# Optimization experiments

Measured on AMD Instinct MI355X. Metric: run time of the kernel, lower is better.

Reference implementation:

```python
import jax, jax.numpy as jnp
import numpy as np

DIM, HEADS = 1024, 16
B, N = 2, 2048


def setup_inputs() -> dict:
    key = jax.random.key(0)
    ks = jax.random.split(key, 8)
    d = DIM // HEADS
    return {
        "x": jax.random.normal(ks[0], (B, N, DIM), dtype=jnp.float32),
        "w_qkv": jax.random.normal(ks[1], (DIM, 3 * DIM), dtype=jnp.float32) * (DIM ** -0.5),
        "w_out": jax.random.normal(ks[2], (DIM, DIM), dtype=jnp.float32) * (DIM ** -0.5),
        "b_out": jnp.zeros((DIM,), dtype=jnp.float32),
        "void_q": jax.random.normal(ks[3], (1, HEADS, 1, d), dtype=jnp.float32),
        "void_k": jax.random.normal(ks[4], (1, HEADS, 1, d), dtype=jnp.float32),
        "void_v": jax.random.normal(ks[5], (1, HEADS, 1, d), dtype=jnp.float32),
        "attention_trace": jax.random.uniform(ks[6], (HEADS, 1, 1), dtype=jnp.float32),
        "temperature_factor": jax.random.normal(ks[7], (HEADS, 1, 1), dtype=jnp.float32),
    }


def reference(x, w_qkv, w_out, b_out, void_q, void_k, void_v,
              attention_trace, temperature_factor):
    b, n, dim = x.shape
    h = void_q.shape[1]
    d = dim // h

    qkv = x @ w_qkv  # [b, n, 3*dim]
    q, k, v = jnp.split(qkv, 3, axis=-1)

    def to_heads(t):
        return t.reshape(b, n, h, d).transpose(0, 2, 1, 3)  # b h n d

    q, k, v = to_heads(q), to_heads(k), to_heads(v)

    # append the void token to q, k, v -> seq length n+1
    q = jnp.concatenate([q, jnp.broadcast_to(void_q, (b, h, 1, d))], axis=2)
    k = jnp.concatenate([k, jnp.broadcast_to(void_k, (b, h, 1, d))], axis=2)
    v = jnp.concatenate([v, jnp.broadcast_to(void_v, (b, h, 1, d))], axis=2)

    # NOTE: original scales by full dim**-0.5, not head-dim
    dots = jnp.einsum('bhid,bhjd->bhij', q, k) * (dim ** -0.5)
    # void-to-void bias of +10 at index [n, n]
    dots = dots.at[:, :, n, n].add(10.0)

    # stateful per-head temperature (trace is a buffer, treated as input)
    temperature = jnp.maximum(1.0 + jnp.abs(attention_trace) * temperature_factor, 1.0)  # [h,1,1]
    attn = jax.nn.softmax(dots / temperature, axis=-1)  # [b, h, n+1, n+1]

    out = jnp.einsum('bhij,bhjd->bhid', attn, v)[:, :, :n, :]  # drop void row
    out = out.transpose(0, 2, 1, 3).reshape(b, n, dim)  # b n (h d)
    return out @ w_out + b_out
```

## Files before the change

### kernel.cpp

```cpp
#include <hip/hip_runtime.h>
#include <stdint.h>

#define DIMF   1024
#define HEADS  16
#define HD     64
#define BB     2
#define NN     2048
#define NKP    2112
#define NTILE  33

typedef __attribute__((ext_vector_type(8))) __bf16 bf16x8;
typedef __attribute__((ext_vector_type(4))) float  f32x4;

__device__ __forceinline__ float b2f(uint16_t h) {
  union { uint32_t u; float f; } v; v.u = ((uint32_t)h) << 16; return v.f;
}
__device__ __forceinline__ uint16_t f2b(float f) {
  union { float f; uint32_t u; } v; v.f = f;
  uint32_t r = v.u + 0x7FFFu + ((v.u >> 16) & 1u);
  return (uint16_t)(r >> 16);
}

__device__ __forceinline__ void gl_lds16(const void* g, void* l) {
  __builtin_amdgcn_global_load_lds(
      (const __attribute__((address_space(1))) void*)g,
      (__attribute__((address_space(3))) void*)l, 16, 0, 0);
}

__global__ __launch_bounds__(256) void prep_k(const float* __restrict__ x,
                                              uint16_t* __restrict__ x_bf,
                                              const float* __restrict__ vk,
                                              const float* __restrict__ vv,
                                              uint16_t* __restrict__ k_ws,
                                              uint16_t* __restrict__ vt_ws) {
  if (blockIdx.x < 4096) {
    int i = blockIdx.x * 256 + threadIdx.x;
    float4 v = *(const float4*)&x[(size_t)i * 4];
    uint16_t* d = x_bf + (size_t)i * 4;
    d[0] = f2b(v.x); d[1] = f2b(v.y); d[2] = f2b(v.z); d[3] = f2b(v.w);
  } else {
    int idx = (blockIdx.x - 4096) * 256 + threadIdx.x;
    int dd = idx & 63;
    int r  = (idx >> 6) & 63;
    int bh = idx >> 12;
    int h  = bh & (HEADS - 1);
    uint16_t kv  = (r == 0) ? f2b(vk[h * HD + dd]) : (uint16_t)0;
    uint16_t vvv = (r == 0) ? f2b(vv[h * HD + dd]) : (uint16_t)0;
    k_ws[((size_t)bh * NKP + NN + r) * HD + dd]  = kv;
    vt_ws[((size_t)bh * HD + dd) * NKP + NN + r] = vvv;
  }
}

__global__ __launch_bounds__(256) void transpose2_k(const float* __restrict__ w1,
                                                    uint16_t* __restrict__ d1,
                                                    const float* __restrict__ w2,
                                                    uint16_t* __restrict__ d2) {
  const int z = blockIdx.z;
  if (z == 1 && blockIdx.x >= 32) return;
  const float* src = z ? w2 : w1;
  uint16_t*   dst = z ? d2 : d1;
  const int M = 1024, N = z ? 1024 : 3072;
  __shared__ uint16_t tile[32][33];
  int bx = blockIdx.x * 32, by = blockIdx.y * 32;
  int x = threadIdx.x & 31, y0 = (threadIdx.x >> 5) * 4;
#pragma unroll
  for (int i = 0; i < 4; ++i)
    tile[y0 + i][x] = f2b(src[(size_t)(by + y0 + i) * N + bx + x]);
  __syncthreads();
#pragma unroll
  for (int i = 0; i < 4; ++i)
    dst[(size_t)(bx + y0 + i) * M + by + x] = tile[x][y0 + i];
}

template<int EPI>
__global__ __launch_bounds__(256) void gemm_bt(const uint16_t* __restrict__ A,
                                               const uint16_t* __restrict__ Bt,
                                               int K, int Nout,
                                               uint16_t* __restrict__ o0,
                                               uint16_t* __restrict__ o1,
                                               uint16_t* __restrict__ o2,
                                               float* __restrict__ fo,
                                               const float* __restrict__ bias) {
  __shared__ uint16_t lds_a[128][32];
  __shared__ uint16_t lds_b[128][32];
  const int m0 = blockIdx.y * 128, n0 = blockIdx.x * 128;
  const int tid = threadIdx.x, lane = tid & 63, wid = tid >> 6;
  const int wm = (wid >> 1) * 64, wn = (wid & 1) * 64;
  const int lr = lane & 15, lg = lane >> 4;
  f32x4 acc[4][4] = {};
  for (int k0 = 0; k0 < K; k0 += 32) {
    __syncthreads();
#pragma unroll
    for (int it = 0; it < 2; ++it) {
      const int chunk = wid * 2 + it;
      const int o = chunk * 1024 + lane * 16;
      const int r = o >> 6, cb = o & 63;
      gl_lds16((const char*)&A[(size_t)(m0 + r) * K + k0] + cb,
               (char*)&lds_a[0][0] + chunk * 1024);
      gl_lds16((const char*)&Bt[(size_t)(n0 + r) * K + k0] + cb,
               (char*)&lds_b[0][0] + chunk * 1024);
    }
    __syncthreads();
    bf16x8 af[4], bf[4];
#pragma unroll
    for (int i = 0; i < 4; ++i)
      af[i] = *(const bf16x8*)((const char*)&lds_a[0][0] + (wm + i * 16 + lr) * 64 + lg * 16);
#pragma unroll
    for (int j = 0; j < 4; ++j)
      bf[j] = *(const bf16x8*)((const char*)&lds_b[0][0] + (wn + j * 16 + lr) * 64 + lg * 16);
#pragma unroll
    for (int i = 0; i < 4; ++i)
#pragma unroll
      for (int j = 0; j < 4; ++j)
        acc[i][j] = __builtin_amdgcn_mfma_f32_16x16x32_bf16(af[i], bf[j], acc[i][j], 0, 0, 0);
  }
#pragma unroll
  for (int i = 0; i < 4; ++i)
#pragma unroll
    for (int j = 0; j < 4; ++j)
#pragma unroll
      for (int r = 0; r < 4; ++r) {
        int mg = m0 + wm + i * 16 + lg * 4 + r;
        int ng = n0 + wn + j * 16 + lr;
        float v = acc[i][j][r];
        if (EPI == 0) {
          int b = mg >> 11, n = mg & (NN - 1);
          int which = ng >> 10, rem = ng & (DIMF - 1), h = rem >> 6, dd = rem & 63;
          int bh = b * HEADS + h;
          uint16_t bv = f2b(v);
          if (which == 0)      o0[((size_t)bh * NN + n) * HD + dd] = bv;
          else if (which == 1) o1[((size_t)bh * NKP + n) * HD + dd] = bv;
          else                 o2[((size_t)bh * HD + dd) * NKP + n] = bv;
        } else {
          fo[(size_t)mg * Nout + ng] = v + bias[ng];
        }
      }
}

__global__ __launch_bounds__(256) void attn_k(const uint16_t* __restrict__ q_ws,
                                              const uint16_t* __restrict__ k_ws,
                                              const uint16_t* __restrict__ vt_ws,
                                              const float* __restrict__ trace,
                                              const float* __restrict__ factor,
                                              uint16_t* __restrict__ o_ws) {
  __shared__ uint16_t ldsk[64][64];
  __shared__ uint16_t ldsv[64][64];
  __shared__ uint16_t ldsp[4][16][72];
  const int bh = blockIdx.x;
  const int qb = blockIdx.y;
  const int h = bh & (HEADS - 1), b = bh >> 4;
  const int tid = threadIdx.x, lane = tid & 63, wid = tid >> 6;
  const int lr = lane & 15, lg = lane >> 4;

  const float temp  = fmaxf(1.0f + fabsf(trace[h]) * factor[h], 1.0f);
  const float scale = 0.03125f / temp;

  const int qrow0 = qb * 64 + wid * 16;
  const uint16_t* qrow = q_ws + ((size_t)bh * NN + qrow0 + lr) * HD;
  bf16x8 qf[2];
  qf[0] = *(const bf16x8*)(qrow + lg * 8);
  qf[1] = *(const bf16x8*)(qrow + 32 + lg * 8);

  const int rsw = (lr & 7) << 4;
  const char* kb0 = (const char*)&ldsk[0][0] + lr * 128 + ((lg * 16) ^ rsw);
  const char* kb1 = (const char*)&ldsk[0][0] + lr * 128 + ((64 + lg * 16) ^ rsw);
  const char* vb0 = (const char*)&ldsv[0][0] + lr * 128 + ((lg * 16) ^ rsw);
  const char* vb1 = (const char*)&ldsv[0][0] + lr * 128 + ((64 + lg * 16) ^ rsw);
  const char* pr  = (const char*)&ldsp[wid][lr][lg * 8];

  f32x4 acc[4] = {};
  float lsum[4] = {0.f, 0.f, 0.f, 0.f};

  for (int t = 0; t < NTILE; ++t) {
    const int t0 = t * 64;
    __syncthreads();
#pragma unroll
    for (int it = 0; it < 2; ++it) {
      const int chunk = wid * 2 + it;
      const int o = chunk * 1024 + lane * 16;
      const int r = o >> 7, cb = o & 127;
      const int scb = cb ^ ((r & 7) << 4);
      gl_lds16((const char*)&k_ws[((size_t)bh * NKP + t0 + r) * HD] + scb,
               (char*)&ldsk[0][0] + chunk * 1024);
      gl_lds16((const char*)&vt_ws[((size_t)bh * HD + r) * NKP + t0] + scb,
               (char*)&ldsv[0][0] + chunk * 1024);
    }
    __syncthreads();

    f32x4 s[4];
#pragma unroll
    for (int c = 0; c < 4; ++c) {
      bf16x8 kf0 = *(const bf16x8*)(kb0 + c * 2048);
      bf16x8 kf1 = *(const bf16x8*)(kb1 + c * 2048);
      f32x4 sa = {};
      __builtin_amdgcn_s_setprio(1);
      sa = __builtin_amdgcn_mfma_f32_16x16x32_bf16(qf[0], kf0, sa, 0, 0, 0);
      sa = __builtin_amdgcn_mfma_f32_16x16x32_bf16(qf[1], kf1, sa, 0, 0, 0);
      __builtin_amdgcn_s_setprio(0);
      s[c] = sa;
    }
#pragma unroll
    for (int c = 0; c < 4; ++c)
#pragma unroll
      for (int r = 0; r < 4; ++r) {
        union { float f; uint32_t u; } pv;
        pv.f = __expf(s[c][r] * scale);
        ldsp[wid][lg * 4 + r][c * 16 + lr] = (uint16_t)(pv.u >> 16);
        pv.u &= 0xffff0000u;
        lsum[r] += pv.f;
      }
    asm volatile("" ::: "memory");
    __builtin_amdgcn_sched_barrier(0);
    __builtin_amdgcn_s_setprio(1);
#pragma unroll
    for (int kk = 0; kk < 2; ++kk) {
      bf16x8 pf = *(const bf16x8*)(pr + kk * 64);
#pragma unroll
      for (int cd = 0; cd < 4; ++cd) {
        bf16x8 vf = *(const bf16x8*)((kk ? vb1 : vb0) + cd * 2048);
        acc[cd] = __builtin_amdgcn_mfma_f32_16x16x32_bf16(pf, vf, acc[cd], 0, 0, 0);
      }
    }
    __builtin_amdgcn_s_setprio(0);
  }
#pragma unroll
  for (int r = 0; r < 4; ++r) {
    float l = lsum[r];
    l += __shfl_xor(l, 1); l += __shfl_xor(l, 2);
    l += __shfl_xor(l, 4); l += __shfl_xor(l, 8);
    l -= 63.0f;
    const float inv = 1.0f / l;
    const int n = qrow0 + lg * 4 + r;
    size_t base = ((size_t)b * NN + n) * DIMF + h * HD;
#pragma unroll
    for (int cd = 0; cd < 4; ++cd)
      o_ws[base + cd * 16 + lr] = f2b(acc[cd][r] * inv);
  }
}

extern "C" void kernel_launch(void* const* d_in, const int* in_sizes, int n_in,
                              void* d_out, int out_size, void* d_ws, size_t ws_size,
                              hipStream_t stream) {
  const float* x      = (const float*)d_in[0];
  const float* wqkv   = (const float*)d_in[1];
  const float* wout   = (const float*)d_in[2];
  const float* bout   = (const float*)d_in[3];
  const float* voidk  = (const float*)d_in[5];
  const float* voidv  = (const float*)d_in[6];
  const float* trace  = (const float*)d_in[7];
  const float* factor = (const float*)d_in[8];
  float* out = (float*)d_out;

  uint16_t* ws    = (uint16_t*)d_ws;
  uint16_t* x_bf  = ws;
  uint16_t* o_ws  = x_bf;
  uint16_t* wqkvT = x_bf  + 4194304;
  uint16_t* woutT = wqkvT + 3145728;
  uint16_t* q_ws  = woutT + 1048576;
  uint16_t* k_ws  = q_ws  + 4194304;
  uint16_t* vt_ws = k_ws  + 4325376;

  prep_k<<<dim3(4608), dim3(256), 0, stream>>>(x, x_bf, voidk, voidv, k_ws, vt_ws);
  transpose2_k<<<dim3(96, 32, 2), dim3(256), 0, stream>>>(wqkv, wqkvT, wout, woutT);
  gemm_bt<0><<<dim3(3072 / 128, 4096 / 128), dim3(256), 0, stream>>>(
      x_bf, wqkvT, 1024, 3072, q_ws, k_ws, vt_ws, nullptr, nullptr);
  attn_k<<<dim3(HEADS * BB, NN / 64), dim3(256), 0, stream>>>(
      q_ws, k_ws, vt_ws, trace, factor, o_ws);
  gemm_bt<1><<<dim3(1024 / 128, 4096 / 128), dim3(256), 0, stream>>>(
      o_ws, woutT, 1024, 1024, nullptr, nullptr, nullptr, out, bout);
}
```

Baseline: 154.1 us.

## Double attention query tile per block and fold weight transpose into prep kernel

The attention kernel now uses 512-thread blocks covering 128 query rows, so each K/V tile loaded into LDS is reused by twice as many query rows and global K/V traffic drops. Each warp now loads a single chunk per tile. Separately, the weight transpose/convert is merged into the prep kernel to save a launch. The trade-off is half as many attention blocks, which may reduce latency hiding, and a larger P scratch buffer in LDS.

```diff
diff --git a/kernel.cpp b/kernel.cpp
--- a/kernel.cpp
+++ b/kernel.cpp
@@ -32,14 +32,20 @@
                                               const float* __restrict__ vk,
                                               const float* __restrict__ vv,
                                               uint16_t* __restrict__ k_ws,
-                                              uint16_t* __restrict__ vt_ws) {
-  if (blockIdx.x < 4096) {
-    int i = blockIdx.x * 256 + threadIdx.x;
+                                              uint16_t* __restrict__ vt_ws,
+                                              const float* __restrict__ wqkv,
+                                              uint16_t* __restrict__ wqkvT,
+                                              const float* __restrict__ wout,
+                                              uint16_t* __restrict__ woutT) {
+  __shared__ uint16_t tile[32][33];
+  const int blk = blockIdx.x;
+  if (blk < 4096) {
+    int i = blk * 256 + threadIdx.x;
     float4 v = *(const float4*)&x[(size_t)i * 4];
     uint16_t* d = x_bf + (size_t)i * 4;
     d[0] = f2b(v.x); d[1] = f2b(v.y); d[2] = f2b(v.z); d[3] = f2b(v.w);
-  } else {
-    int idx = (blockIdx.x - 4096) * 256 + threadIdx.x;
+  } else if (blk < 4608) {
+    int idx = (blk - 4096) * 256 + threadIdx.x;
     int dd = idx & 63;
     int r  = (idx >> 6) & 63;
     int bh = idx >> 12;
@@ -48,28 +54,21 @@
     uint16_t vvv = (r == 0) ? f2b(vv[h * HD + dd]) : (uint16_t)0;
     k_ws[((size_t)bh * NKP + NN + r) * HD + dd]  = kv;
     vt_ws[((size_t)bh * HD + dd) * NKP + NN + r] = vvv;
-  }
-}
-
-__global__ __launch_bounds__(256) void transpose2_k(const float* __restrict__ w1,
-                                                    uint16_t* __restrict__ d1,
-                                                    const float* __restrict__ w2,
-                                                    uint16_t* __restrict__ d2) {
-  const int z = blockIdx.z;
-  if (z == 1 && blockIdx.x >= 32) return;
-  const float* src = z ? w2 : w1;
-  uint16_t*   dst = z ? d2 : d1;
-  const int M = 1024, N = z ? 1024 : 3072;
-  __shared__ uint16_t tile[32][33];
-  int bx = blockIdx.x * 32, by = blockIdx.y * 32;
-  int x = threadIdx.x & 31, y0 = (threadIdx.x >> 5) * 4;
-#pragma unroll
-  for (int i = 0; i < 4; ++i)
-    tile[y0 + i][x] = f2b(src[(size_t)(by + y0 + i) * N + bx + x]);
-  __syncthreads();
-#pragma unroll
-  for (int i = 0; i < 4; ++i)
-    dst[(size_t)(bx + y0 + i) * M + by + x] = tile[x][y0 + i];
+  } else {
+    int tb = blk - 4608;
+    const float* src; uint16_t* dst; int N, bx, by;
+    if (tb < 3072) { src = wqkv; dst = wqkvT; N = 3072; bx = (tb % 96) * 32; by = (tb / 96) * 32; }
+    else { tb -= 3072; src = wout; dst = woutT; N = 1024; bx = (tb % 32) * 32; by = (tb / 32) * 32; }
+    const int M = 1024;
+    int xx = threadIdx.x & 31, y0 = (threadIdx.x >> 5) * 4;
+#pragma unroll
+    for (int i = 0; i < 4; ++i)
+      tile[y0 + i][xx] = f2b(src[(size_t)(by + y0 + i) * N + bx + xx]);
+    __syncthreads();
+#pragma unroll
+    for (int i = 0; i < 4; ++i)
+      dst[(size_t)(bx + y0 + i) * M + by + xx] = tile[xx][y0 + i];
+  }
 }
 
 template<int EPI>
@@ -137,7 +136,7 @@
       }
 }
 
-__global__ __launch_bounds__(256) void attn_k(const uint16_t* __restrict__ q_ws,
+__global__ __launch_bounds__(512) void attn_k(const uint16_t* __restrict__ q_ws,
                                               const uint16_t* __restrict__ k_ws,
                                               const uint16_t* __restrict__ vt_ws,
                                               const float* __restrict__ trace,
@@ -145,7 +144,7 @@
                                               uint16_t* __restrict__ o_ws) {
   __shared__ uint16_t ldsk[64][64];
   __shared__ uint16_t ldsv[64][64];
-  __shared__ uint16_t ldsp[4][16][72];
+  __shared__ uint16_t ldsp[8][16][72];
   const int bh = blockIdx.x;
   const int qb = blockIdx.y;
   const int h = bh & (HEADS - 1), b = bh >> 4;
@@ -155,7 +154,7 @@
   const float temp  = fmaxf(1.0f + fabsf(trace[h]) * factor[h], 1.0f);
   const float scale = 0.03125f / temp;
 
-  const int qrow0 = qb * 64 + wid * 16;
+  const int qrow0 = qb * 128 + wid * 16;
   const uint16_t* qrow = q_ws + ((size_t)bh * NN + qrow0 + lr) * HD;
   bf16x8 qf[2];
   qf[0] = *(const bf16x8*)(qrow + lg * 8);
@@ -174,9 +173,8 @@
   for (int t = 0; t < NTILE; ++t) {
     const int t0 = t * 64;
     __syncthreads();
-#pragma unroll
-    for (int it = 0; it < 2; ++it) {
-      const int chunk = wid * 2 + it;
+    {
+      const int chunk = wid;
       const int o = chunk * 1024 + lane * 16;
       const int r = o >> 7, cb = o & 127;
       const int scb = cb ^ ((r & 7) << 4);
@@ -260,11 +258,11 @@
   uint16_t* k_ws  = q_ws  + 4194304;
   uint16_t* vt_ws = k_ws  + 4325376;
 
-  prep_k<<<dim3(4608), dim3(256), 0, stream>>>(x, x_bf, voidk, voidv, k_ws, vt_ws);
-  transpose2_k<<<dim3(96, 32, 2), dim3(256), 0, stream>>>(wqkv, wqkvT, wout, woutT);
+  prep_k<<<dim3(8704), dim3(256), 0, stream>>>(x, x_bf, voidk, voidv, k_ws, vt_ws,
+                                               wqkv, wqkvT, wout, woutT);
   gemm_bt<0><<<dim3(3072 / 128, 4096 / 128), dim3(256), 0, stream>>>(
       x_bf, wqkvT, 1024, 3072, q_ws, k_ws, vt_ws, nullptr, nullptr);
-  attn_k<<<dim3(HEADS * BB, NN / 64), dim3(256), 0, stream>>>(
+  attn_k<<<dim3(HEADS * BB, NN / 128), dim3(512), 0, stream>>>(
       q_ws, k_ws, vt_ws, trace, factor, o_ws);
   gemm_bt<1><<<dim3(1024 / 128, 4096 / 128), dim3(256), 0, stream>>>(
       o_ws, woutT, 1024, 1024, nullptr, nullptr, nullptr, out, bout);
```

Result: faster. 138.7 us (-10.0%).
